# Kernel tuning notes

Measured on AMD Instinct MI355X. Metric: run time of the kernel, lower is better.

Reference implementation:

```python
import jax, jax.numpy as jnp
from jax import lax
import numpy as np

B, N, D = 64, 1025, 384   # tokens = 1 CLS + 32x32 patch grid
G = 32
K = 8                      # num rotation bases
KS = 8                     # num scale bases
R = 8                      # rank of skew bases
H = 128                    # controller hidden dim
CIN = 3 * D                # cls_mean_var pooling
OUT = D
ROT_GATE_BIAS = -4.0
LOCAL_GATE_BIAS = -3.0


def setup_inputs() -> dict:
    key = jax.random.key(0)
    ks = jax.random.split(key, 16)
    f32 = jnp.float32
    inp = {
        "x": jax.random.normal(ks[0], (B, N, D), f32),
        "shared_weight": jax.random.normal(ks[1], (OUT, D), f32) * 0.02,
        "bias": jnp.zeros((OUT,), f32),
        "left_basis": jax.random.normal(ks[2], (K, D, R), f32) * 0.02,
        "right_basis": jax.random.normal(ks[3], (K, D, R), f32) * 0.02,
        "scale_basis": jax.random.normal(ks[4], (KS, OUT), f32) * 0.01,
        "scale_strength": jnp.asarray(0.25, f32),
        "dw_kernel": jax.random.normal(ks[5], (D, 1, 3, 3), f32) * 0.1,  # depthwise 3x3
        "ctrl_w1": jax.random.normal(ks[6], (H, CIN), f32) * 0.02,
        "ctrl_b1": jnp.zeros((H,), f32),
        "w_rot": jax.random.normal(ks[7], (K, H), f32) * 0.02,
        "b_rot": jnp.zeros((K,), f32),
        "w_rgate": jax.random.normal(ks[8], (1, H), f32) * 0.02,
        "b_rgate": jnp.full((1,), ROT_GATE_BIAS, f32),
        "w_lgate": jax.random.normal(ks[9], (1, H), f32) * 0.02,
        "b_lgate": jnp.full((1,), LOCAL_GATE_BIAS, f32),
        "w_scale": jax.random.normal(ks[10], (KS, H), f32) * 0.02,
        "b_scale": jnp.zeros((KS,), f32),
    }
    return inp


def _forward(x, shared_weight, bias, left_basis, right_basis, scale_basis,
             scale_strength, dw_kernel, ctrl_w1, ctrl_b1, w_rot, b_rot,
             w_rgate, b_rgate, w_lgate, b_lgate, w_scale, b_scale):
    b, n, d = x.shape
    # --- conditioning signal: cls | mean | var (unbiased=False) ---
    cls = x[:, 0]
    mean = jnp.mean(x, axis=1)
    var = jnp.var(x, axis=1)
    z = jnp.concatenate([cls, mean, var], axis=-1)          # [B, 3D]
    # --- controller MLP ---
    h = jax.nn.gelu(z @ ctrl_w1.T + ctrl_b1)                 # [B, H]
    rot_coeff = jnp.tanh(h @ w_rot.T + b_rot)                # [B, K]
    rot_gate = jax.nn.sigmoid(h @ w_rgate.T + b_rgate)[:, 0] # [B]
    local_gate = jax.nn.sigmoid(h @ w_lgate.T + b_lgate)[:, 0]
    scale_coeff = jnp.tanh(h @ w_scale.T + b_scale)          # [B, KS]
    # --- gated local depthwise-conv mixer on the patch grid ---
    cls_tok = x[:, :1, :]
    patch = x[:, 1:, :]                                      # [B, G*G, D]
    grid = patch.transpose(0, 2, 1).reshape(b, d, G, G)      # NCHW
    local = lax.conv_general_dilated(
        grid, dw_kernel, window_strides=(1, 1), padding="SAME",
        feature_group_count=d, dimension_numbers=("NCHW", "OIHW", "NCHW"))
    local_tok = local.reshape(b, d, G * G).transpose(0, 2, 1)
    mixed_patch = patch + local_gate[:, None, None] * (local_tok - patch)
    lm = jnp.concatenate([cls_tok, mixed_patch], axis=1)     # [B, N, D]
    # --- normalized skew bases from low-rank factors ---
    basis = (jnp.einsum("kdr,ker->kde", left_basis, right_basis)
             - jnp.einsum("kdr,ker->kde", right_basis, left_basis))  # [K, D, D]
    norm = jnp.maximum(jnp.linalg.norm(basis.reshape(K, -1), axis=1), 1e-6)
    basis = basis / norm[:, None, None]
    # --- per-sample Cayley rotation (fp32 solve) ---
    skew = jnp.einsum("bk,kde->bde", rot_coeff, basis)       # residual_scale = 1.0
    eye = jnp.eye(d, dtype=jnp.float32)
    half = 0.5 * skew
    transform = jnp.linalg.solve(eye - half, jnp.broadcast_to(eye, half.shape) + half)
    transform = transform.astype(x.dtype)
    # --- gated rotation of features ---
    rotated = jnp.einsum("bnd,bdh->bnh", lm, transform)
    mixed = lm + rot_gate[:, None, None] * (rotated - lm)
    # --- shared linear + dynamic output scaling ---
    preact = mixed @ shared_weight.T + bias                  # [B, N, OUT]
    scale_delta = jnp.tanh(scale_coeff @ scale_basis)        # [B, OUT]
    scale = 1.0 + scale_strength * scale_delta[:, None, :]
    return preact * scale


def reference(x, shared_weight, bias, left_basis, right_basis, scale_basis,
              scale_strength, dw_kernel, ctrl_w1, ctrl_b1, w_rot, b_rot,
              w_rgate, b_rgate, w_lgate, b_lgate, w_scale, b_scale):
    return _forward(x, shared_weight, bias, left_basis, right_basis, scale_basis,
                    scale_strength, dw_kernel, ctrl_w1, ctrl_b1, w_rot, b_rot,
                    w_rgate, b_rgate, w_lgate, b_lgate, w_scale, b_scale)
```

## Files before the change

kernel.cpp:

```cpp
#include <hip/hip_runtime.h>
#include <hip/hip_bf16.h>
#include <math.h>

static const int Bb = 64, Nn = 1025, Dd = 384, Kk = 8, Rr = 8, Hh = 128, CINc = 1152, OUTo = 384;

#define OFF_PSTAT 0u
#define OFF_RC    475136u
#define OFF_RG    475648u
#define OFF_LG    475712u
#define OFF_SCALE 476288u
#define OFF_N2    505472u
#define OFF_P     505600u
#define OFF_Q     554752u
#define OFF_G     603904u
#define OFF_QW    620288u
#define OFF_PB    669440u
#define OFF_EP    694016u
#define OFF_ZT    3839744u
#define OFF_WBT   5412608u
#define OFF_LM    10131200u

typedef __attribute__((ext_vector_type(8))) short short8;
typedef __attribute__((ext_vector_type(8))) __bf16 bf16x8;
typedef __attribute__((ext_vector_type(4))) float f32x4;

#define MFMA_BF16(a,b,c) __builtin_amdgcn_mfma_f32_16x16x32_bf16( \
    __builtin_bit_cast(bf16x8,(a)), __builtin_bit_cast(bf16x8,(b)), (c), 0, 0, 0)

#define GLDS16(gp, lp) __builtin_amdgcn_global_load_lds( \
    (__attribute__((address_space(1))) void*)(gp), \
    (__attribute__((address_space(3))) void*)(lp), 16, 0, 0)

__device__ __forceinline__ float gelu_t(float v){
    float u = 0.7978845608028654f*(v + 0.044715f*v*v*v);
    return 0.5f*v*(1.0f + tanhf(u));
}
__device__ __forceinline__ float sigm(float v){ return 1.0f/(1.0f+expf(-v)); }
__device__ __forceinline__ unsigned short f2bf(float v){
    return __builtin_bit_cast(unsigned short, __float2bfloat16(v));
}

__global__ __launch_bounds__(384) void k_stats(const float* __restrict__ x, float* __restrict__ ps){
    int s = blockIdx.x, b = blockIdx.y, t = threadIdx.x;
    int dq = t % 96, ng = t / 96;
    int n0 = s*129, n1 = n0+129 < Nn ? n0+129 : Nn;
    const float4* xb = (const float4*)(x + (size_t)b*Nn*Dd);
    float4 sm = make_float4(0.f,0.f,0.f,0.f), sq = make_float4(0.f,0.f,0.f,0.f);
    for (int n = n0+ng; n < n1; n += 4){
        float4 v = xb[(size_t)n*96 + dq];
        sm.x += v.x; sm.y += v.y; sm.z += v.z; sm.w += v.w;
        sq.x += v.x*v.x; sq.y += v.y*v.y; sq.z += v.z*v.z; sq.w += v.w*v.w;
    }
    __shared__ float4 smS[384];
    __shared__ float4 sqS[384];
    smS[t] = sm; sqS[t] = sq;
    __syncthreads();
    if (t < 96){
        float4 a0 = smS[t], a1 = smS[t+96], a2 = smS[t+192], a3 = smS[t+288];
        float4 q0 = sqS[t], q1 = sqS[t+96], q2 = sqS[t+192], q3 = sqS[t+288];
        float4 a = make_float4(a0.x+a1.x+a2.x+a3.x, a0.y+a1.y+a2.y+a3.y, a0.z+a1.z+a2.z+a3.z, a0.w+a1.w+a2.w+a3.w);
        float4 q = make_float4(q0.x+q1.x+q2.x+q3.x, q0.y+q1.y+q2.y+q3.y, q0.z+q1.z+q2.z+q3.z, q0.w+q1.w+q2.w+q3.w);
        ((float4*)(ps + ((size_t)(b*8+s)*2+0)*Dd))[t] = a;
        ((float4*)(ps + ((size_t)(b*8+s)*2+1)*Dd))[t] = q;
    }
}

__global__ __launch_bounds__(384) void k_ctrl(const float* __restrict__ x, const float* __restrict__ ps,
    const float* __restrict__ w1, const float* __restrict__ b1,
    const float* __restrict__ w_rot, const float* __restrict__ b_rot,
    const float* __restrict__ w_rg, const float* __restrict__ b_rg,
    const float* __restrict__ w_lg, const float* __restrict__ b_lg,
    const float* __restrict__ w_sc, const float* __restrict__ b_sc,
    const float* __restrict__ sbasis, const float* __restrict__ sstr,
    float* __restrict__ rc, float* __restrict__ rg, float* __restrict__ lg,
    float* __restrict__ scalev, unsigned short* __restrict__ lm){
    __shared__ float zs[1152];
    __shared__ float hp[3*128];
    __shared__ float hs[128];
    __shared__ float scl[8];
    int b = blockIdx.x, t = threadIdx.x;
    float sm = 0.f, sq = 0.f;
    for (int s = 0; s < 8; ++s){
        sm += ps[((size_t)(b*8+s)*2+0)*Dd + t];
        sq += ps[((size_t)(b*8+s)*2+1)*Dd + t];
    }
    float mean = sm*(1.0f/Nn);
    float var  = sq*(1.0f/Nn) - mean*mean;
    float cls  = x[(size_t)b*Nn*Dd + t];
    zs[t] = cls; zs[Dd + t] = mean; zs[2*Dd + t] = var;
    lm[(size_t)b*Nn*Dd + t] = f2bf(cls);
    __syncthreads();
    {
        int row = t & 127, part = t >> 7;
        const float* wrow = w1 + (size_t)row*CINc + part*384;
        const float* zp = zs + part*384;
        float acc = 0.f;
        for (int c = 0; c < 384; ++c) acc += zp[c]*wrow[c];
        hp[part*128 + row] = acc;
    }
    __syncthreads();
    if (t < 128)
        hs[t] = gelu_t(hp[t] + hp[128+t] + hp[256+t] + b1[t]);
    __syncthreads();
    if (t < 8){
        float acc = b_rot[t]; const float* w = w_rot + (size_t)t*Hh;
        for (int c = 0; c < Hh; ++c) acc += hs[c]*w[c];
        rc[b*8+t] = tanhf(acc);
    } else if (t == 8){
        float acc = b_rg[0];
        for (int c = 0; c < Hh; ++c) acc += hs[c]*w_rg[c];
        rg[b] = sigm(acc);
    } else if (t == 9){
        float acc = b_lg[0];
        for (int c = 0; c < Hh; ++c) acc += hs[c]*w_lg[c];
        lg[b] = sigm(acc);
    } else if (t < 18){
        int q = t-10; float acc = b_sc[q]; const float* w = w_sc + (size_t)q*Hh;
        for (int c = 0; c < Hh; ++c) acc += hs[c]*w[c];
        scl[q] = tanhf(acc);
    }
    __syncthreads();
    float acc = 0.f;
    #pragma unroll
    for (int q = 0; q < 8; ++q) acc += scl[q]*sbasis[q*OUTo + t];
    scalev[(size_t)b*OUTo + t] = 1.0f + sstr[0]*tanhf(acc);
}

__global__ __launch_bounds__(256) void k_prep(const float* __restrict__ lb, const float* __restrict__ rb,
                                              float* __restrict__ n2, float* __restrict__ P,
                                              float* __restrict__ Q, unsigned short* __restrict__ Pb){
    int bid = blockIdx.x, t = threadIdx.x;
    if (bid < 8){
        if (t < 64){
            int k = bid;
            int r = t >> 3, s = t & 7;
            const float* L = lb + (size_t)k*Dd*Rr;
            const float* R = rb + (size_t)k*Dd*Rr;
            float a = 0.f, bsum = 0.f, c = 0.f, c2 = 0.f;
            for (int d = 0; d < Dd; ++d){
                float lr = L[d*8+r], ls = L[d*8+s], rr = R[d*8+r], rs = R[d*8+s];
                a += lr*ls; bsum += rr*rs; c += lr*rs; c2 += ls*rr;
            }
            float contrib = a*bsum - c*c2;
            for (int m = 32; m > 0; m >>= 1) contrib += __shfl_xor(contrib, m, 64);
            if (t == 0) n2[k] = 2.f*contrib;
        }
    } else {
        int idx = (bid-8)*256 + t;
        int d = idx >> 7, j = idx & 127;
        int k = (j & 63) >> 3, r = j & 7;
        float lv = lb[((size_t)k*Dd + d)*Rr + r];
        float rv = rb[((size_t)k*Dd + d)*Rr + r];
        float pv = (j < 64) ? lv : rv;
        P[idx] = pv;
        Pb[idx] = f2bf(pv);
        Q[idx] = (j < 64) ? rv : lv;
    }
}

__global__ __launch_bounds__(512) void k_gramqw(const float* __restrict__ P, const float* __restrict__ Q,
                                                const float* __restrict__ Wsh,
                                                float* __restrict__ G, float* __restrict__ QW){
    __shared__ float qc[384];
    int i = blockIdx.x, t = threadIdx.x;
    for (int d = t; d < Dd; d += 512) qc[d] = Q[d*128 + i];
    __syncthreads();
    if (t < 128){
        float a = 0.f;
        for (int d = 0; d < Dd; ++d) a += qc[d]*P[d*128 + t];
        G[i*128 + t] = a;
    } else {
        int o = t - 128;
        float a = 0.f;
        const float* wrow = Wsh + (size_t)o*Dd;
        for (int d = 0; d < Dd; ++d) a += qc[d]*wrow[d];
        QW[(size_t)i*OUTo + o] = a;
    }
}

__global__ __launch_bounds__(512) void k_cayley(const float* __restrict__ G, const float* __restrict__ rc,
                                                const float* __restrict__ n2, const float* __restrict__ rg,
                                                float* __restrict__ Ep){
    __shared__ float GT[128*128];
    __shared__ float Xs[128*128];
    int b = blockIdx.x, t = threadIdx.x;
    for (int lin = t; lin < 16384; lin += 512){
        int i = lin >> 7, m = lin & 127;
        GT[m*128 + i] = G[lin];
    }
    int j0 = (t & 15)*8, i0 = (t >> 4)*4;
    float dj[8], di[4];
    #pragma unroll
    for (int u = 0; u < 8; ++u){
        int j = j0+u; int k = (j&63)>>3;
        float nrm = fmaxf(sqrtf(n2[k]), 1e-6f);
        float al = 0.5f*rc[b*8+k]/nrm;
        dj[u] = (j < 64) ? al : -al;
    }
    #pragma unroll
    for (int u = 0; u < 4; ++u){
        int i = i0+u; int k = (i&63)>>3;
        float nrm = fmaxf(sqrtf(n2[k]), 1e-6f);
        float al = 0.5f*rc[b*8+k]/nrm;
        di[u] = (i < 64) ? al : -al;
    }
    __syncthreads();
    float B0[4][8], acc[4][8];
    #pragma unroll
    for (int ui = 0; ui < 4; ++ui)
        #pragma unroll
        for (int uj = 0; uj < 8; ++uj){
            int i = i0+ui, j = j0+uj;
            float g = GT[j*128 + i];
            B0[ui][uj] = di[ui]*g*dj[uj] + ((i==j) ? di[ui] : 0.f);
        }
    #pragma unroll
    for (int ui = 0; ui < 4; ++ui)
        #pragma unroll
        for (int uj = 0; uj < 8; ++uj)
            Xs[(i0+ui)*128 + j0+uj] = B0[ui][uj];
    __syncthreads();
    for (int pass = 0; pass < 2; ++pass){
        #pragma unroll
        for (int ui = 0; ui < 4; ++ui)
            #pragma unroll
            for (int uj = 0; uj < 8; ++uj) acc[ui][uj] = 0.f;
        for (int m = 0; m < 128; ++m){
            float4 g4 = *(const float4*)&GT[m*128 + i0];
            float4 xa = *(const float4*)&Xs[m*128 + j0];
            float4 xb = *(const float4*)&Xs[m*128 + j0 + 4];
            float gi[4] = {g4.x, g4.y, g4.z, g4.w};
            float xv[8] = {xa.x, xa.y, xa.z, xa.w, xb.x, xb.y, xb.z, xb.w};
            #pragma unroll
            for (int ui = 0; ui < 4; ++ui)
                #pragma unroll
                for (int uj = 0; uj < 8; ++uj)
                    acc[ui][uj] += gi[ui]*xv[uj];
        }
        if (pass == 0){
            __syncthreads();
            #pragma unroll
            for (int ui = 0; ui < 4; ++ui)
                #pragma unroll
                for (int uj = 0; uj < 8; ++uj)
                    Xs[(i0+ui)*128 + j0+uj] = B0[ui][uj] + di[ui]*acc[ui][uj];
            __syncthreads();
        }
    }
    float rgb = rg[b];
    #pragma unroll
    for (int ui = 0; ui < 4; ++ui){
        int i = i0+ui;
        float o[8];
        #pragma unroll
        for (int uj = 0; uj < 8; ++uj){
            int j = j0+uj;
            float x2 = B0[ui][uj] + di[ui]*acc[ui][uj];
            o[uj] = rgb*(x2 + ((i==j) ? di[ui] : 0.f));
        }
        float4* ep4 = (float4*)(Ep + ((size_t)b*128 + i)*128 + j0);
        ep4[0] = make_float4(o[0], o[1], o[2], o[3]);
        ep4[1] = make_float4(o[4], o[5], o[6], o[7]);
    }
}

__global__ __launch_bounds__(384) void k_zmatT(const float* __restrict__ Ep, const float* __restrict__ QW, unsigned short* __restrict__ ZT){
    __shared__ float Es[4*128];
    int ig = blockIdx.x, b = blockIdx.y, t = threadIdx.x;
    int i0 = ig*4;
    for (int lin = t; lin < 512; lin += 384)
        Es[lin] = Ep[((size_t)b*128 + i0 + (lin >> 7))*128 + (lin & 127)];
    __syncthreads();
    float a0=0.f, a1=0.f, a2=0.f, a3=0.f;
    for (int m = 0; m < 128; ++m){
        float qw = QW[(size_t)m*OUTo + t];
        a0 += Es[m]*qw; a1 += Es[128+m]*qw; a2 += Es[256+m]*qw; a3 += Es[384+m]*qw;
    }
    ushort4 uv;
    uv.x = f2bf(a0); uv.y = f2bf(a1); uv.z = f2bf(a2); uv.w = f2bf(a3);
    *(ushort4*)(ZT + ((size_t)b*OUTo + t)*128 + i0) = uv;
}

__global__ __launch_bounds__(256) void k_wbt(const unsigned short* __restrict__ ZT, const unsigned short* __restrict__ Pb,
                                             const float* __restrict__ Wsh, unsigned short* __restrict__ WbT){
    __shared__ short8 As[256];
    __shared__ short8 Bs[256];
    int b = blockIdx.y;
    int mt = blockIdx.x/6, nt2 = blockIdx.x%6;
    int m0 = mt*64, n0 = nt2*64;
    int t = threadIdx.x;
    int w = t>>6, l = t&63;
    int wr = w>>1, wc = w&1;
    const unsigned short* Ab = ZT + (size_t)b*OUTo*128;
    int lrow = t>>2, lseg = t&3;
    f32x4 acc[2][2];
    #pragma unroll
    for (int mi=0;mi<2;++mi)
        #pragma unroll
        for (int ni=0;ni<2;++ni)
            #pragma unroll
            for (int q=0;q<4;++q) acc[mi][ni][q] = 0.f;
    for (int kt = 0; kt < 4; ++kt){
        int k0 = kt*32;
        short8 av = *(const short8*)(Ab + (size_t)(m0+lrow)*128 + k0 + lseg*8);
        short8 bv = *(const short8*)(Pb + (size_t)(n0+lrow)*128 + k0 + lseg*8);
        __syncthreads();
        As[lseg*64 + lrow] = av;
        Bs[lseg*64 + lrow] = bv;
        __syncthreads();
        short8 a0 = As[(l>>4)*64 + wr*32 + (l&15)];
        short8 a1 = As[(l>>4)*64 + wr*32 + 16 + (l&15)];
        short8 b0 = Bs[(l>>4)*64 + wc*32 + (l&15)];
        short8 b1 = Bs[(l>>4)*64 + wc*32 + 16 + (l&15)];
        acc[0][0] = MFMA_BF16(a0, b0, acc[0][0]);
        acc[0][1] = MFMA_BF16(a0, b1, acc[0][1]);
        acc[1][0] = MFMA_BF16(a1, b0, acc[1][0]);
        acc[1][1] = MFMA_BF16(a1, b1, acc[1][1]);
    }
    unsigned short* Wo = WbT + (size_t)b*OUTo*Dd;
    #pragma unroll
    for (int mi=0;mi<2;++mi){
        #pragma unroll
        for (int ni=0;ni<2;++ni){
            int col = n0 + wc*32 + ni*16 + (l&15);
            #pragma unroll
            for (int r=0;r<4;++r){
                int row = m0 + wr*32 + mi*16 + (l>>4)*4 + r;
                float v = Wsh[(size_t)row*Dd + col] + acc[mi][ni][r];
                Wo[(size_t)row*Dd + col] = f2bf(v);
            }
        }
    }
}

__global__ __launch_bounds__(384) void k_lm(const float* __restrict__ x, const float* __restrict__ kw,
                                            const float* __restrict__ lg, unsigned short* __restrict__ lm){
    __shared__ float kws[9*384];
    int flat = blockIdx.x;
    int work = (flat & 7)*256 + (flat >> 3);
    int b = work >> 5, gy = work & 31;
    int t = threadIdx.x;
    for (int i = t; i < 3456; i += 384){
        int d = i % 384, tap = i / 384;
        kws[tap*384 + d] = kw[d*9 + tap];
    }
    __syncthreads();
    int dq = t % 96, gxg = t / 96;
    float lgb = lg[b];
    const float4* xb = (const float4*)(x + (size_t)b*Nn*Dd);
    unsigned short* lmb = lm + (size_t)b*Nn*Dd;
    #pragma unroll
    for (int u = 0; u < 8; ++u){
        int gx = gxg + 4*u;
        int n = 1 + (gy << 5) + gx;
        float4 xc = xb[(size_t)n*96 + dq];
        float ax = 0.f, ay = 0.f, az = 0.f, aw = 0.f;
        #pragma unroll
        for (int ky = 0; ky < 3; ++ky){
            int yy = gy + ky - 1;
            if ((unsigned)yy < 32u){
                #pragma unroll
                for (int kx = 0; kx < 3; ++kx){
                    int xx = gx + kx - 1;
                    if ((unsigned)xx < 32u){
                        float4 xv = xb[(size_t)(1 + (yy << 5) + xx)*96 + dq];
                        const float4 kv = *(const float4*)(&kws[(ky*3+kx)*384 + dq*4]);
                        ax += xv.x*kv.x; ay += xv.y*kv.y; az += xv.z*kv.z; aw += xv.w*kv.w;
                    }
                }
            }
        }
        ushort4 o4;
        o4.x = f2bf(xc.x + lgb*(ax - xc.x));
        o4.y = f2bf(xc.y + lgb*(ay - xc.y));
        o4.z = f2bf(xc.z + lgb*(az - xc.z));
        o4.w = f2bf(xc.w + lgb*(aw - xc.w));
        *(ushort4*)(lmb + (size_t)n*Dd + dq*4) = o4;
    }
}

__global__ __launch_bounds__(256) void k_gemm_nt(const unsigned short* __restrict__ lm, const unsigned short* __restrict__ WbT,
                                                 const float* __restrict__ bias, const float* __restrict__ scalev,
                                                 float* __restrict__ out){
    __shared__ unsigned short smem[24576];
    __shared__ float svs[128];
    __shared__ float bvs[128];
    int flat = blockIdx.x;
    int work = (flat & 7)*216 + (flat >> 3);
    int b = work / 27;
    int r = work - b*27;
    int nt = r / 3, ot = r - nt*3;
    int n0 = nt*128, o0 = ot*128;
    int t = threadIdx.x;
    int w = t >> 6, l = t & 63;
    int wr = w >> 1, wc = w & 1;
    const unsigned short* Ab = lm + (size_t)b*Nn*Dd;
    const unsigned short* Bt = WbT + (size_t)b*OUTo*Dd;
    if (t < 128){ svs[t] = scalev[(size_t)b*OUTo + o0 + t]; bvs[t] = bias[o0 + t]; }
    int srow = l >> 2;
    int gch  = (l & 3) ^ ((l >> 3) & 3);
    f32x4 acc[4][4];
    #pragma unroll
    for (int fi = 0; fi < 4; ++fi)
        #pragma unroll
        for (int fj = 0; fj < 4; ++fj)
            #pragma unroll
            for (int q = 0; q < 4; ++q) acc[fi][fj][q] = 0.f;

#define STG(bufi, k0) { \
    unsigned short* Adst = &smem[(bufi)*8192 + (w*32)*32]; \
    unsigned short* Bdst = &smem[(bufi)*8192 + 4096 + (w*32)*32]; \
    GLDS16(Ab + (size_t)(n0 + w*32 + srow)*Dd + (k0) + gch*8, Adst); \
    GLDS16(Ab + (size_t)(n0 + w*32 + 16 + srow)*Dd + (k0) + gch*8, Adst + 512); \
    GLDS16(Bt + (size_t)(o0 + w*32 + srow)*Dd + (k0) + gch*8, Bdst); \
    GLDS16(Bt + (size_t)(o0 + w*32 + 16 + srow)*Dd + (k0) + gch*8, Bdst + 512); }

    STG(0, 0);
    STG(1, 32);
    int rch = ((l>>4) ^ (((l&15)>>1)&3)) * 8;
    int raBase = (wr*64 + (l&15))*32;
    int rbBase = (wc*64 + (l&15))*32;
    for (int kt = 0; kt < 12; ++kt){
        if (kt < 10) STG((kt+2)%3, (kt+2)*32);
        if (kt < 10)       asm volatile("s_waitcnt vmcnt(8)" ::: "memory");
        else if (kt == 10) asm volatile("s_waitcnt vmcnt(4)" ::: "memory");
        else               asm volatile("s_waitcnt vmcnt(0)" ::: "memory");
        __builtin_amdgcn_s_barrier();
        __builtin_amdgcn_sched_barrier(0);
        const unsigned short* As  = &smem[(kt%3)*8192];
        const unsigned short* Bs2 = &smem[(kt%3)*8192 + 4096];
        short8 a[4], bb[4];
        #pragma unroll
        for (int f = 0; f < 4; ++f){
            a[f]  = *(const short8*)&As [raBase + f*512 + rch];
            bb[f] = *(const short8*)&Bs2[rbBase + f*512 + rch];
        }
        #pragma unroll
        for (int fi = 0; fi < 4; ++fi)
            #pragma unroll
            for (int fj = 0; fj < 4; ++fj)
                acc[fi][fj] = MFMA_BF16(a[fi], bb[fj], acc[fi][fj]);
        __builtin_amdgcn_sched_barrier(0);
        __builtin_amdgcn_s_barrier();
    }
#undef STG
    float* Cs = (float*)smem;
    #pragma unroll
    for (int h = 0; h < 2; ++h){
        __syncthreads();
        if (wr == h){
            #pragma unroll
            for (int fi = 0; fi < 4; ++fi)
                #pragma unroll
                for (int fj = 0; fj < 4; ++fj){
                    int col = wc*64 + fj*16 + (l&15);
                    #pragma unroll
                    for (int q = 0; q < 4; ++q){
                        int row = fi*16 + (l>>4)*4 + q;
                        Cs[row*132 + col] = acc[fi][fj][q];
                    }
                }
        }
        __syncthreads();
        #pragma unroll
        for (int p = 0; p < 8; ++p){
            int idx = p*256 + t;
            int row = idx >> 5, c4 = idx & 31;
            int gr = n0 + h*64 + row;
            if (gr < Nn){
                float4 v = *(const float4*)&Cs[row*132 + c4*4];
                float4 o4;
                o4.x = svs[c4*4+0]*(bvs[c4*4+0] + v.x);
                o4.y = svs[c4*4+1]*(bvs[c4*4+1] + v.y);
                o4.z = svs[c4*4+2]*(bvs[c4*4+2] + v.z);
                o4.w = svs[c4*4+3]*(bvs[c4*4+3] + v.w);
                *(float4*)(out + ((size_t)b*Nn + gr)*OUTo + o0 + c4*4) = o4;
            }
        }
    }
}

extern "C" void kernel_launch(void* const* d_in, const int* in_sizes, int n_in,
                              void* d_out, int out_size, void* d_ws, size_t ws_size,
                              hipStream_t stream){
    const float* x     = (const float*)d_in[0];
    const float* Wsh   = (const float*)d_in[1];
    const float* bias  = (const float*)d_in[2];
    const float* lb    = (const float*)d_in[3];
    const float* rb    = (const float*)d_in[4];
    const float* sbasis= (const float*)d_in[5];
    const float* sstr  = (const float*)d_in[6];
    const float* kw    = (const float*)d_in[7];
    const float* w1    = (const float*)d_in[8];
    const float* b1    = (const float*)d_in[9];
    const float* w_rot = (const float*)d_in[10];
    const float* b_rot = (const float*)d_in[11];
    const float* w_rg  = (const float*)d_in[12];
    const float* b_rg  = (const float*)d_in[13];
    const float* w_lg  = (const float*)d_in[14];
    const float* b_lg  = (const float*)d_in[15];
    const float* w_sc  = (const float*)d_in[16];
    const float* b_sc  = (const float*)d_in[17];
    float* out = (float*)d_out;
    float* ws  = (float*)d_ws;

    float* ps     = ws + OFF_PSTAT;
    float* rc     = ws + OFF_RC;
    float* rg     = ws + OFF_RG;
    float* lg     = ws + OFF_LG;
    float* scalev = ws + OFF_SCALE;
    float* n2     = ws + OFF_N2;
    float* P      = ws + OFF_P;
    float* Q      = ws + OFF_Q;
    float* G      = ws + OFF_G;
    float* QW     = ws + OFF_QW;
    unsigned short* Pb  = (unsigned short*)(ws + OFF_PB);
    float* Ep     = ws + OFF_EP;
    unsigned short* ZT  = (unsigned short*)(ws + OFF_ZT);
    unsigned short* WbT = (unsigned short*)(ws + OFF_WBT);
    unsigned short* lmb = (unsigned short*)(ws + OFF_LM);

    k_stats   <<<dim3(8, Bb), 384, 0, stream>>>(x, ps);
    k_ctrl    <<<Bb, 384, 0, stream>>>(x, ps, w1, b1, w_rot, b_rot, w_rg, b_rg, w_lg, b_lg,
                                       w_sc, b_sc, sbasis, sstr, rc, rg, lg, scalev, lmb);
    k_prep    <<<200, 256, 0, stream>>>(lb, rb, n2, P, Q, Pb);
    k_gramqw  <<<128, 512, 0, stream>>>(P, Q, Wsh, G, QW);
    k_cayley  <<<Bb, 512, 0, stream>>>(G, rc, n2, rg, Ep);
    k_zmatT   <<<dim3(32, Bb), 384, 0, stream>>>(Ep, QW, ZT);
    k_wbt     <<<dim3(36, Bb), 256, 0, stream>>>(ZT, Pb, Wsh, WbT);
    k_lm      <<<2048, 384, 0, stream>>>(x, kw, lg, lmb);
    k_gemm_nt <<<1728, 256, 0, stream>>>(lmb, WbT, bias, scalev, out);
}
```

Before: 261.3 us.

## Merge independent small kernels into fewer launches and quad-buffer GEMM staging

Independent stages are merged into shared launches selected by block index: stats with basis prep, controller MLP with gram/QW, and the depthwise conv with the zmat product. This cuts the launch count from nine to six and lets independent work overlap inside one grid. The GEMM moves from three to four LDS staging buffers so the trailing barrier in each k-step can be dropped. The extra LDS per block may lower occupancy. The fused kernels also take the larger shared-memory and register footprint of their combined branches.

```diff
diff --git a/kernel.cpp b/kernel.cpp
--- a/kernel.cpp
+++ b/kernel.cpp
@@ -40,105 +40,43 @@
     return __builtin_bit_cast(unsigned short, __float2bfloat16(v));
 }
 
-__global__ __launch_bounds__(384) void k_stats(const float* __restrict__ x, float* __restrict__ ps){
-    int s = blockIdx.x, b = blockIdx.y, t = threadIdx.x;
-    int dq = t % 96, ng = t / 96;
-    int n0 = s*129, n1 = n0+129 < Nn ? n0+129 : Nn;
-    const float4* xb = (const float4*)(x + (size_t)b*Nn*Dd);
-    float4 sm = make_float4(0.f,0.f,0.f,0.f), sq = make_float4(0.f,0.f,0.f,0.f);
-    for (int n = n0+ng; n < n1; n += 4){
-        float4 v = xb[(size_t)n*96 + dq];
-        sm.x += v.x; sm.y += v.y; sm.z += v.z; sm.w += v.w;
-        sq.x += v.x*v.x; sq.y += v.y*v.y; sq.z += v.z*v.z; sq.w += v.w*v.w;
-    }
-    __shared__ float4 smS[384];
-    __shared__ float4 sqS[384];
-    smS[t] = sm; sqS[t] = sq;
-    __syncthreads();
-    if (t < 96){
-        float4 a0 = smS[t], a1 = smS[t+96], a2 = smS[t+192], a3 = smS[t+288];
-        float4 q0 = sqS[t], q1 = sqS[t+96], q2 = sqS[t+192], q3 = sqS[t+288];
-        float4 a = make_float4(a0.x+a1.x+a2.x+a3.x, a0.y+a1.y+a2.y+a3.y, a0.z+a1.z+a2.z+a3.z, a0.w+a1.w+a2.w+a3.w);
-        float4 q = make_float4(q0.x+q1.x+q2.x+q3.x, q0.y+q1.y+q2.y+q3.y, q0.z+q1.z+q2.z+q3.z, q0.w+q1.w+q2.w+q3.w);
-        ((float4*)(ps + ((size_t)(b*8+s)*2+0)*Dd))[t] = a;
-        ((float4*)(ps + ((size_t)(b*8+s)*2+1)*Dd))[t] = q;
-    }
-}
-
-__global__ __launch_bounds__(384) void k_ctrl(const float* __restrict__ x, const float* __restrict__ ps,
-    const float* __restrict__ w1, const float* __restrict__ b1,
-    const float* __restrict__ w_rot, const float* __restrict__ b_rot,
-    const float* __restrict__ w_rg, const float* __restrict__ b_rg,
-    const float* __restrict__ w_lg, const float* __restrict__ b_lg,
-    const float* __restrict__ w_sc, const float* __restrict__ b_sc,
-    const float* __restrict__ sbasis, const float* __restrict__ sstr,
-    float* __restrict__ rc, float* __restrict__ rg, float* __restrict__ lg,
-    float* __restrict__ scalev, unsigned short* __restrict__ lm){
-    __shared__ float zs[1152];
-    __shared__ float hp[3*128];
-    __shared__ float hs[128];
-    __shared__ float scl[8];
-    int b = blockIdx.x, t = threadIdx.x;
-    float sm = 0.f, sq = 0.f;
-    for (int s = 0; s < 8; ++s){
-        sm += ps[((size_t)(b*8+s)*2+0)*Dd + t];
-        sq += ps[((size_t)(b*8+s)*2+1)*Dd + t];
-    }
-    float mean = sm*(1.0f/Nn);
-    float var  = sq*(1.0f/Nn) - mean*mean;
-    float cls  = x[(size_t)b*Nn*Dd + t];
-    zs[t] = cls; zs[Dd + t] = mean; zs[2*Dd + t] = var;
-    lm[(size_t)b*Nn*Dd + t] = f2bf(cls);
-    __syncthreads();
-    {
-        int row = t & 127, part = t >> 7;
-        const float* wrow = w1 + (size_t)row*CINc + part*384;
-        const float* zp = zs + part*384;
-        float acc = 0.f;
-        for (int c = 0; c < 384; ++c) acc += zp[c]*wrow[c];
-        hp[part*128 + row] = acc;
-    }
-    __syncthreads();
-    if (t < 128)
-        hs[t] = gelu_t(hp[t] + hp[128+t] + hp[256+t] + b1[t]);
-    __syncthreads();
-    if (t < 8){
-        float acc = b_rot[t]; const float* w = w_rot + (size_t)t*Hh;
-        for (int c = 0; c < Hh; ++c) acc += hs[c]*w[c];
-        rc[b*8+t] = tanhf(acc);
-    } else if (t == 8){
-        float acc = b_rg[0];
-        for (int c = 0; c < Hh; ++c) acc += hs[c]*w_rg[c];
-        rg[b] = sigm(acc);
-    } else if (t == 9){
-        float acc = b_lg[0];
-        for (int c = 0; c < Hh; ++c) acc += hs[c]*w_lg[c];
-        lg[b] = sigm(acc);
-    } else if (t < 18){
-        int q = t-10; float acc = b_sc[q]; const float* w = w_sc + (size_t)q*Hh;
-        for (int c = 0; c < Hh; ++c) acc += hs[c]*w[c];
-        scl[q] = tanhf(acc);
-    }
-    __syncthreads();
-    float acc = 0.f;
-    #pragma unroll
-    for (int q = 0; q < 8; ++q) acc += scl[q]*sbasis[q*OUTo + t];
-    scalev[(size_t)b*OUTo + t] = 1.0f + sstr[0]*tanhf(acc);
-}
-
-__global__ __launch_bounds__(256) void k_prep(const float* __restrict__ lb, const float* __restrict__ rb,
-                                              float* __restrict__ n2, float* __restrict__ P,
-                                              float* __restrict__ Q, unsigned short* __restrict__ Pb){
+__global__ __launch_bounds__(384) void k_statsprep(const float* __restrict__ x,
+    const float* __restrict__ lb, const float* __restrict__ rb,
+    float* __restrict__ ps, float* __restrict__ n2,
+    float* __restrict__ P, float* __restrict__ Q, unsigned short* __restrict__ Pb){
     int bid = blockIdx.x, t = threadIdx.x;
-    if (bid < 8){
+    if (bid < 512){
+        int s = bid & 7, b = bid >> 3;
+        int dq = t % 96, ng = t / 96;
+        int n0 = s*129, n1 = n0+129 < Nn ? n0+129 : Nn;
+        const float4* xb = (const float4*)(x + (size_t)b*Nn*Dd);
+        float4 sm = make_float4(0.f,0.f,0.f,0.f), sq = make_float4(0.f,0.f,0.f,0.f);
+        for (int n = n0+ng; n < n1; n += 4){
+            float4 v = xb[(size_t)n*96 + dq];
+            sm.x += v.x; sm.y += v.y; sm.z += v.z; sm.w += v.w;
+            sq.x += v.x*v.x; sq.y += v.y*v.y; sq.z += v.z*v.z; sq.w += v.w*v.w;
+        }
+        __shared__ float4 smS[384];
+        __shared__ float4 sqS[384];
+        smS[t] = sm; sqS[t] = sq;
+        __syncthreads();
+        if (t < 96){
+            float4 a0 = smS[t], a1 = smS[t+96], a2 = smS[t+192], a3 = smS[t+288];
+            float4 q0 = sqS[t], q1 = sqS[t+96], q2 = sqS[t+192], q3 = sqS[t+288];
+            float4 a = make_float4(a0.x+a1.x+a2.x+a3.x, a0.y+a1.y+a2.y+a3.y, a0.z+a1.z+a2.z+a3.z, a0.w+a1.w+a2.w+a3.w);
+            float4 q = make_float4(q0.x+q1.x+q2.x+q3.x, q0.y+q1.y+q2.y+q3.y, q0.z+q1.z+q2.z+q3.z, q0.w+q1.w+q2.w+q3.w);
+            ((float4*)(ps + ((size_t)(b*8+s)*2+0)*Dd))[t] = a;
+            ((float4*)(ps + ((size_t)(b*8+s)*2+1)*Dd))[t] = q;
+        }
+    } else if (bid < 520){
         if (t < 64){
-            int k = bid;
-            int r = t >> 3, s = t & 7;
+            int k = bid - 512;
+            int r = t >> 3, s2 = t & 7;
             const float* L = lb + (size_t)k*Dd*Rr;
             const float* R = rb + (size_t)k*Dd*Rr;
             float a = 0.f, bsum = 0.f, c = 0.f, c2 = 0.f;
             for (int d = 0; d < Dd; ++d){
-                float lr = L[d*8+r], ls = L[d*8+s], rr = R[d*8+r], rs = R[d*8+s];
+                float lr = L[d*8+r], ls = L[d*8+s2], rr = R[d*8+r], rs = R[d*8+s2];
                 a += lr*ls; bsum += rr*rs; c += lr*rs; c2 += ls*rr;
             }
             float contrib = a*bsum - c*c2;
@@ -146,7 +84,7 @@
             if (t == 0) n2[k] = 2.f*contrib;
         }
     } else {
-        int idx = (bid-8)*256 + t;
+        int idx = (bid - 520)*384 + t;
         int d = idx >> 7, j = idx & 127;
         int k = (j & 63) >> 3, r = j & 7;
         float lv = lb[((size_t)k*Dd + d)*Rr + r];
@@ -158,23 +96,89 @@
     }
 }
 
-__global__ __launch_bounds__(512) void k_gramqw(const float* __restrict__ P, const float* __restrict__ Q,
-                                                const float* __restrict__ Wsh,
-                                                float* __restrict__ G, float* __restrict__ QW){
-    __shared__ float qc[384];
-    int i = blockIdx.x, t = threadIdx.x;
-    for (int d = t; d < Dd; d += 512) qc[d] = Q[d*128 + i];
-    __syncthreads();
-    if (t < 128){
-        float a = 0.f;
-        for (int d = 0; d < Dd; ++d) a += qc[d]*P[d*128 + t];
-        G[i*128 + t] = a;
+__global__ __launch_bounds__(512) void k_ctrlgram(const float* __restrict__ x, const float* __restrict__ ps,
+    const float* __restrict__ w1, const float* __restrict__ b1,
+    const float* __restrict__ w_rot, const float* __restrict__ b_rot,
+    const float* __restrict__ w_rg, const float* __restrict__ b_rg,
+    const float* __restrict__ w_lg, const float* __restrict__ b_lg,
+    const float* __restrict__ w_sc, const float* __restrict__ b_sc,
+    const float* __restrict__ sbasis, const float* __restrict__ sstr,
+    const float* __restrict__ P, const float* __restrict__ Q, const float* __restrict__ Wsh,
+    float* __restrict__ rc, float* __restrict__ rg, float* __restrict__ lg,
+    float* __restrict__ scalev, unsigned short* __restrict__ lm,
+    float* __restrict__ G, float* __restrict__ QW){
+    int bid = blockIdx.x, t = threadIdx.x;
+    if (bid < 128){
+        __shared__ float qc[384];
+        int i = bid;
+        for (int d = t; d < Dd; d += 512) qc[d] = Q[d*128 + i];
+        __syncthreads();
+        if (t < 128){
+            float a = 0.f;
+            for (int d = 0; d < Dd; ++d) a += qc[d]*P[d*128 + t];
+            G[i*128 + t] = a;
+        } else {
+            int o = t - 128;
+            float a = 0.f;
+            const float* wrow = Wsh + (size_t)o*Dd;
+            for (int d = 0; d < Dd; ++d) a += qc[d]*wrow[d];
+            QW[(size_t)i*OUTo + o] = a;
+        }
     } else {
-        int o = t - 128;
-        float a = 0.f;
-        const float* wrow = Wsh + (size_t)o*Dd;
-        for (int d = 0; d < Dd; ++d) a += qc[d]*wrow[d];
-        QW[(size_t)i*OUTo + o] = a;
+        __shared__ float zs[1152];
+        __shared__ float hp[4*128];
+        __shared__ float hs[128];
+        __shared__ float scl[8];
+        int b = bid - 128;
+        if (t < 384){
+            float sm = 0.f, sq = 0.f;
+            for (int s = 0; s < 8; ++s){
+                sm += ps[((size_t)(b*8+s)*2+0)*Dd + t];
+                sq += ps[((size_t)(b*8+s)*2+1)*Dd + t];
+            }
+            float mean = sm*(1.0f/Nn);
+            float var  = sq*(1.0f/Nn) - mean*mean;
+            float cls  = x[(size_t)b*Nn*Dd + t];
+            zs[t] = cls; zs[Dd + t] = mean; zs[2*Dd + t] = var;
+            lm[(size_t)b*Nn*Dd + t] = f2bf(cls);
+        }
+        __syncthreads();
+        {
+            int row = t & 127, part = t >> 7;
+            const float* wrow = w1 + (size_t)row*CINc + part*288;
+            const float* zp = zs + part*288;
+            float acc = 0.f;
+            for (int c = 0; c < 288; ++c) acc += zp[c]*wrow[c];
+            hp[part*128 + row] = acc;
+        }
+        __syncthreads();
+        if (t < 128)
+            hs[t] = gelu_t(hp[t] + hp[128+t] + hp[256+t] + hp[384+t] + b1[t]);
+        __syncthreads();
+        if (t < 8){
+            float acc = b_rot[t]; const float* w = w_rot + (size_t)t*Hh;
+            for (int c = 0; c < Hh; ++c) acc += hs[c]*w[c];
+            rc[b*8+t] = tanhf(acc);
+        } else if (t == 8){
+            float acc = b_rg[0];
+            for (int c = 0; c < Hh; ++c) acc += hs[c]*w_rg[c];
+            rg[b] = sigm(acc);
+        } else if (t == 9){
+            float acc = b_lg[0];
+            for (int c = 0; c < Hh; ++c) acc += hs[c]*w_lg[c];
+            lg[b] = sigm(acc);
+        } else if (t < 18){
+            int q = t-10; float acc = b_sc[q]; const float* w = w_sc + (size_t)q*Hh;
+            for (int c = 0; c < Hh; ++c) acc += hs[c]*w[c];
+            scl[q] = tanhf(acc);
+        }
+        __syncthreads();
+        if (t < 384){
+            float acc = 0.f;
+            #pragma unroll
+            for (int q = 0; q < 8; ++q) acc += scl[q]*sbasis[q*OUTo + t];
+            scalev[(size_t)b*OUTo + t] = 1.0f + sstr[0]*tanhf(acc);
+        }
     }
 }
 
@@ -264,21 +268,69 @@
     }
 }
 
-__global__ __launch_bounds__(384) void k_zmatT(const float* __restrict__ Ep, const float* __restrict__ QW, unsigned short* __restrict__ ZT){
-    __shared__ float Es[4*128];
-    int ig = blockIdx.x, b = blockIdx.y, t = threadIdx.x;
-    int i0 = ig*4;
-    for (int lin = t; lin < 512; lin += 384)
-        Es[lin] = Ep[((size_t)b*128 + i0 + (lin >> 7))*128 + (lin & 127)];
-    __syncthreads();
-    float a0=0.f, a1=0.f, a2=0.f, a3=0.f;
-    for (int m = 0; m < 128; ++m){
-        float qw = QW[(size_t)m*OUTo + t];
-        a0 += Es[m]*qw; a1 += Es[128+m]*qw; a2 += Es[256+m]*qw; a3 += Es[384+m]*qw;
-    }
-    ushort4 uv;
-    uv.x = f2bf(a0); uv.y = f2bf(a1); uv.z = f2bf(a2); uv.w = f2bf(a3);
-    *(ushort4*)(ZT + ((size_t)b*OUTo + t)*128 + i0) = uv;
+__global__ __launch_bounds__(384) void k_zmlm(const float* __restrict__ x, const float* __restrict__ kw,
+    const float* __restrict__ lg, const float* __restrict__ Ep, const float* __restrict__ QW,
+    unsigned short* __restrict__ lm, unsigned short* __restrict__ ZT){
+    int bid = blockIdx.x, t = threadIdx.x;
+    if (bid < 2048){
+        __shared__ float kws[9*384];
+        int flat = bid;
+        int work = (flat & 7)*256 + (flat >> 3);
+        int b = work >> 5, gy = work & 31;
+        for (int i = t; i < 3456; i += 384){
+            int d = i % 384, tap = i / 384;
+            kws[tap*384 + d] = kw[d*9 + tap];
+        }
+        __syncthreads();
+        int dq = t % 96, gxg = t / 96;
+        float lgb = lg[b];
+        const float4* xb = (const float4*)(x + (size_t)b*Nn*Dd);
+        unsigned short* lmb = lm + (size_t)b*Nn*Dd;
+        #pragma unroll
+        for (int u = 0; u < 8; ++u){
+            int gx = gxg + 4*u;
+            int n = 1 + (gy << 5) + gx;
+            float4 xc = xb[(size_t)n*96 + dq];
+            float ax = 0.f, ay = 0.f, az = 0.f, aw = 0.f;
+            #pragma unroll
+            for (int ky = 0; ky < 3; ++ky){
+                int yy = gy + ky - 1;
+                if ((unsigned)yy < 32u){
+                    #pragma unroll
+                    for (int kx = 0; kx < 3; ++kx){
+                        int xx = gx + kx - 1;
+                        if ((unsigned)xx < 32u){
+                            float4 xv = xb[(size_t)(1 + (yy << 5) + xx)*96 + dq];
+                            const float4 kv = *(const float4*)(&kws[(ky*3+kx)*384 + dq*4]);
+                            ax += xv.x*kv.x; ay += xv.y*kv.y; az += xv.z*kv.z; aw += xv.w*kv.w;
+                        }
+                    }
+                }
+            }
+            ushort4 o4;
+            o4.x = f2bf(xc.x + lgb*(ax - xc.x));
+            o4.y = f2bf(xc.y + lgb*(ay - xc.y));
+            o4.z = f2bf(xc.z + lgb*(az - xc.z));
+            o4.w = f2bf(xc.w + lgb*(aw - xc.w));
+            *(ushort4*)(lmb + (size_t)n*Dd + dq*4) = o4;
+        }
+    } else {
+        __shared__ float Es[4*128];
+        int z = bid - 2048;
+        int ig = z & 31, b = z >> 5;
+        int i0 = ig*4;
+        for (int lin = t; lin < 512; lin += 384)
+            Es[lin] = Ep[((size_t)b*128 + i0 + (lin >> 7))*128 + (lin & 127)];
+        __syncthreads();
+        float a0=0.f, a1=0.f, a2=0.f, a3=0.f;
+        for (int m = 0; m < 128; ++m){
+            float qw = QW[(size_t)m*OUTo + t];
+            a0 += Es[m]*qw; a1 += Es[128+m]*qw; a2 += Es[256+m]*qw; a3 += Es[384+m]*qw;
+        }
+        ushort4 uv;
+        uv.x = f2bf(a0); uv.y = f2bf(a1); uv.z = f2bf(a2); uv.w = f2bf(a3);
+        *(ushort4*)(ZT + ((size_t)b*OUTo + t)*128 + i0) = uv;
+    }
 }
 
 __global__ __launch_bounds__(256) void k_wbt(const unsigned short* __restrict__ ZT, const unsigned short* __restrict__ Pb,
@@ -333,56 +385,10 @@
     }
 }
 
-__global__ __launch_bounds__(384) void k_lm(const float* __restrict__ x, const float* __restrict__ kw,
-                                            const float* __restrict__ lg, unsigned short* __restrict__ lm){
-    __shared__ float kws[9*384];
-    int flat = blockIdx.x;
-    int work = (flat & 7)*256 + (flat >> 3);
-    int b = work >> 5, gy = work & 31;
-    int t = threadIdx.x;
-    for (int i = t; i < 3456; i += 384){
-        int d = i % 384, tap = i / 384;
-        kws[tap*384 + d] = kw[d*9 + tap];
-    }
-    __syncthreads();
-    int dq = t % 96, gxg = t / 96;
-    float lgb = lg[b];
-    const float4* xb = (const float4*)(x + (size_t)b*Nn*Dd);
-    unsigned short* lmb = lm + (size_t)b*Nn*Dd;
-    #pragma unroll
-    for (int u = 0; u < 8; ++u){
-        int gx = gxg + 4*u;
-        int n = 1 + (gy << 5) + gx;
-        float4 xc = xb[(size_t)n*96 + dq];
-        float ax = 0.f, ay = 0.f, az = 0.f, aw = 0.f;
-        #pragma unroll
-        for (int ky = 0; ky < 3; ++ky){
-            int yy = gy + ky - 1;
-            if ((unsigned)yy < 32u){
-                #pragma unroll
-                for (int kx = 0; kx < 3; ++kx){
-                    int xx = gx + kx - 1;
-                    if ((unsigned)xx < 32u){
-                        float4 xv = xb[(size_t)(1 + (yy << 5) + xx)*96 + dq];
-                        const float4 kv = *(const float4*)(&kws[(ky*3+kx)*384 + dq*4]);
-                        ax += xv.x*kv.x; ay += xv.y*kv.y; az += xv.z*kv.z; aw += xv.w*kv.w;
-                    }
-                }
-            }
-        }
-        ushort4 o4;
-        o4.x = f2bf(xc.x + lgb*(ax - xc.x));
-        o4.y = f2bf(xc.y + lgb*(ay - xc.y));
-        o4.z = f2bf(xc.z + lgb*(az - xc.z));
-        o4.w = f2bf(xc.w + lgb*(aw - xc.w));
-        *(ushort4*)(lmb + (size_t)n*Dd + dq*4) = o4;
-    }
-}
-
 __global__ __launch_bounds__(256) void k_gemm_nt(const unsigned short* __restrict__ lm, const unsigned short* __restrict__ WbT,
                                                  const float* __restrict__ bias, const float* __restrict__ scalev,
                                                  float* __restrict__ out){
-    __shared__ unsigned short smem[24576];
+    __shared__ unsigned short smem[32768];
     __shared__ float svs[128];
     __shared__ float bvs[128];
     int flat = blockIdx.x;
@@ -421,14 +427,14 @@
     int raBase = (wr*64 + (l&15))*32;
     int rbBase = (wc*64 + (l&15))*32;
     for (int kt = 0; kt < 12; ++kt){
-        if (kt < 10) STG((kt+2)%3, (kt+2)*32);
+        if (kt < 10) STG((kt+2)&3, (kt+2)*32);
         if (kt < 10)       asm volatile("s_waitcnt vmcnt(8)" ::: "memory");
         else if (kt == 10) asm volatile("s_waitcnt vmcnt(4)" ::: "memory");
         else               asm volatile("s_waitcnt vmcnt(0)" ::: "memory");
         __builtin_amdgcn_s_barrier();
         __builtin_amdgcn_sched_barrier(0);
-        const unsigned short* As  = &smem[(kt%3)*8192];
-        const unsigned short* Bs2 = &smem[(kt%3)*8192 + 4096];
+        const unsigned short* As  = &smem[(kt&3)*8192];
+        const unsigned short* Bs2 = &smem[(kt&3)*8192 + 4096];
         short8 a[4], bb[4];
         #pragma unroll
         for (int f = 0; f < 4; ++f){
@@ -440,8 +446,6 @@
             #pragma unroll
             for (int fj = 0; fj < 4; ++fj)
                 acc[fi][fj] = MFMA_BF16(a[fi], bb[fj], acc[fi][fj]);
-        __builtin_amdgcn_sched_barrier(0);
-        __builtin_amdgcn_s_barrier();
     }
 #undef STG
     float* Cs = (float*)smem;
@@ -520,14 +524,12 @@
     unsigned short* WbT = (unsigned short*)(ws + OFF_WBT);
     unsigned short* lmb = (unsigned short*)(ws + OFF_LM);
 
-    k_stats   <<<dim3(8, Bb), 384, 0, stream>>>(x, ps);
-    k_ctrl    <<<Bb, 384, 0, stream>>>(x, ps, w1, b1, w_rot, b_rot, w_rg, b_rg, w_lg, b_lg,
-                                       w_sc, b_sc, sbasis, sstr, rc, rg, lg, scalev, lmb);
-    k_prep    <<<200, 256, 0, stream>>>(lb, rb, n2, P, Q, Pb);
-    k_gramqw  <<<128, 512, 0, stream>>>(P, Q, Wsh, G, QW);
-    k_cayley  <<<Bb, 512, 0, stream>>>(G, rc, n2, rg, Ep);
-    k_zmatT   <<<dim3(32, Bb), 384, 0, stream>>>(Ep, QW, ZT);
-    k_wbt     <<<dim3(36, Bb), 256, 0, stream>>>(ZT, Pb, Wsh, WbT);
-    k_lm      <<<2048, 384, 0, stream>>>(x, kw, lg, lmb);
-    k_gemm_nt <<<1728, 256, 0, stream>>>(lmb, WbT, bias, scalev, out);
-}
+    k_statsprep<<<648, 384, 0, stream>>>(x, lb, rb, ps, n2, P, Q, Pb);
+    k_ctrlgram <<<192, 512, 0, stream>>>(x, ps, w1, b1, w_rot, b_rot, w_rg, b_rg, w_lg, b_lg,
+                                         w_sc, b_sc, sbasis, sstr, P, Q, Wsh,
+                                         rc, rg, lg, scalev, lmb, G, QW);
+    k_cayley   <<<Bb, 512, 0, stream>>>(G, rc, n2, rg, Ep);
+    k_zmlm     <<<4096, 384, 0, stream>>>(x, kw, lg, Ep, QW, lmb, ZT);
+    k_wbt      <<<dim3(36, Bb), 256, 0, stream>>>(ZT, Pb, Wsh, WbT);
+    k_gemm_nt  <<<1728, 256, 0, stream>>>(lmb, WbT, bias, scalev, out);
+}
```

Result: faster. 224.3 us (-14.2%).
